# Kernel optimization log

Hardware: AMD Instinct MI355X
Metric: run time of the kernel (lower is better)

## Reference

```python
import jax, jax.numpy as jnp
import numpy as np

B, N, P_FEATS = 8, 4096, 3
WIDTH, HEADS, LAYERS, N_LAT = 768, 12, 8, 256
NUM_FREQS = 8
D_HEAD = WIDTH // HEADS
SCALE = 1.0 / np.sqrt(np.sqrt(D_HEAD))  # applied to q and k separately
IN_DIM = 3 * (1 + 2 * NUM_FREQS) + P_FEATS  # 54
EPS = 1e-5


def fourier_embed(pc):
    # pc: [B,N,3] -> [B,N,51] (include_input + sin/cos at freqs 2^0..2^7)
    freqs = (2.0 ** jnp.arange(NUM_FREQS)).astype(pc.dtype)
    ang = pc[..., None] * freqs  # [B,N,3,F]
    ang = ang.reshape(*pc.shape[:-1], 3 * NUM_FREQS)
    return jnp.concatenate([pc, jnp.sin(ang), jnp.cos(ang)], axis=-1)


def layernorm(x, s, b):
    mu = jnp.mean(x, axis=-1, keepdims=True)
    var = jnp.mean(jnp.square(x - mu), axis=-1, keepdims=True)
    return (x - mu) * jax.lax.rsqrt(var + EPS) * s + b


def mh_attn(q, k, v):
    # q: [B,T,H,C], k/v: [B,S,H,C]
    w = jnp.einsum('bthc,bshc->bhts', q * SCALE, k * SCALE)
    w = jax.nn.softmax(w.astype(jnp.float32), axis=-1).astype(q.dtype)
    out = jnp.einsum('bhts,bshc->bthc', w, v)
    return out.reshape(*q.shape[:2], -1)


def setup_inputs() -> dict:
    key = jax.random.key(0)
    ks = iter(jax.random.split(key, 64))
    rn = lambda shape, std=0.02: jax.random.normal(next(ks), shape, jnp.float32) * std
    inp = {
        'pc': jax.random.normal(next(ks), (B, N, 3), jnp.float32),
        'feats': jax.random.uniform(next(ks), (B, N, P_FEATS), jnp.float32),
        'query': rn((N_LAT, WIDTH)),
        'in_W': rn((WIDTH, IN_DIM)), 'in_b': jnp.zeros((WIDTH,)),
        'ca_qkv_W': rn((3 * WIDTH, WIDTH)), 'ca_qkv_b': jnp.zeros((3 * WIDTH,)),
        'ca_proj_W': rn((WIDTH, WIDTH)), 'ca_proj_b': jnp.zeros((WIDTH,)),
        'ln1_s': jnp.ones((LAYERS, WIDTH)), 'ln1_b': jnp.zeros((LAYERS, WIDTH)),
        'qkv_W': rn((LAYERS, 3 * WIDTH, WIDTH)), 'qkv_b': jnp.zeros((LAYERS, 3 * WIDTH)),
        'proj_W': rn((LAYERS, WIDTH, WIDTH)), 'proj_b': jnp.zeros((LAYERS, WIDTH)),
        'ln2_s': jnp.ones((LAYERS, WIDTH)), 'ln2_b': jnp.zeros((LAYERS, WIDTH)),
        'fc_W': rn((LAYERS, 4 * WIDTH, WIDTH)), 'fc_b': jnp.zeros((LAYERS, 4 * WIDTH)),
        'fc2_W': rn((LAYERS, WIDTH, 4 * WIDTH)), 'fc2_b': jnp.zeros((LAYERS, WIDTH)),
    }
    return inp


def _forward(pc, feats, query, in_W, in_b, ca_qkv_W, ca_qkv_b, ca_proj_W, ca_proj_b,
             ln1_s, ln1_b, qkv_W, qkv_b, proj_W, proj_b, ln2_s, ln2_b,
             fc_W, fc_b, fc2_W, fc2_b):
    bs = pc.shape[0]
    data = jnp.concatenate([fourier_embed(pc), feats], axis=-1)  # [B,N,54]
    data = data @ in_W.T + in_b  # [B,N,W]
    q_lat = jnp.broadcast_to(query[None], (bs, N_LAT, WIDTH))

    # --- cross attention (no residual, matching source) ---
    q = (q_lat @ ca_qkv_W.T + ca_qkv_b)[..., :WIDTH]
    kv = data @ ca_qkv_W.T + ca_qkv_b
    k, v = kv[..., WIDTH:2 * WIDTH], kv[..., 2 * WIDTH:]
    q = q.reshape(bs, N_LAT, HEADS, D_HEAD)
    k = k.reshape(bs, N, HEADS, D_HEAD)
    v = v.reshape(bs, N, HEADS, D_HEAD)
    latents = mh_attn(q, k, v) @ ca_proj_W.T + ca_proj_b  # [B,L,W]

    # --- self-attention transformer stack via scan ---
    def block(x, p):
        (l1s, l1b, qW, qb, pW, pb, l2s, l2b, fW, fb, f2W, f2b) = p
        h = layernorm(x, l1s, l1b)
        qkv = (h @ qW.T + qb).reshape(bs, N_LAT, HEADS, 3 * D_HEAD)
        qh, kh, vh = jnp.split(qkv, 3, axis=-1)
        x = x + mh_attn(qh, kh, vh) @ pW.T + pb
        h = layernorm(x, l2s, l2b)
        h = jax.nn.gelu(h @ fW.T + fb, approximate=False) @ f2W.T + f2b
        return x + h, None

    params = (ln1_s, ln1_b, qkv_W, qkv_b, proj_W, proj_b, ln2_s, ln2_b, fc_W, fc_b, fc2_W, fc2_b)
    latents, _ = jax.lax.scan(block, latents, params)
    return latents, pc


def reference(pc, feats, query, in_W, in_b, ca_qkv_W, ca_qkv_b, ca_proj_W, ca_proj_b,
              ln1_s, ln1_b, qkv_W, qkv_b, proj_W, proj_b, ln2_s, ln2_b,
              fc_W, fc_b, fc2_W, fc2_b):
    return _forward(pc, feats, query, in_W, in_b, ca_qkv_W, ca_qkv_b, ca_proj_W, ca_proj_b,
                    ln1_s, ln1_b, qkv_W, qkv_b, proj_W, proj_b, ln2_s, ln2_b,
                    fc_W, fc_b, fc2_W, fc2_b)
```

## Files before the change

kernel.cpp:

```cpp
#include <hip/hip_runtime.h>
#include <stdint.h>

typedef unsigned short u16;
typedef __bf16 bf16x8 __attribute__((ext_vector_type(8)));
typedef float f32x4 __attribute__((ext_vector_type(4)));

#define DEVINL __device__ __forceinline__

DEVINL u16 f2bf(float f) {
  union { float f; unsigned u; } c; c.f = f;
  unsigned u = c.u + 0x7FFFu + ((c.u >> 16) & 1u);
  return (u16)(u >> 16);
}

DEVINL float bf2f(u16 v) {
  union { unsigned u; float f; } c; c.u = (unsigned)v << 16;
  return c.f;
}

DEVINL unsigned pk2bf(float a, float b) {
#if __has_builtin(__builtin_amdgcn_cvt_pk_bf16_f32)
  auto r = __builtin_amdgcn_cvt_pk_bf16_f32(a, b);
  unsigned u;
  __builtin_memcpy(&u, &r, 4);
  return u;
#else
  return (unsigned)f2bf(a) | ((unsigned)f2bf(b) << 16);
#endif
}

DEVINL void gl2lds16(const void* g, void* l) {
  __builtin_amdgcn_global_load_lds(
      (const __attribute__((address_space(1))) unsigned int*)g,
      (__attribute__((address_space(3))) unsigned int*)l, 16, 0, 0);
}

DEVINL void waitlgkm0() { asm volatile("s_waitcnt lgkmcnt(0)" ::: "memory"); }
DEVINL void bar() {
  asm volatile("" ::: "memory");
  __builtin_amdgcn_s_barrier();
  asm volatile("" ::: "memory");
}

__global__ __launch_bounds__(256) void cvt4_kernel(
    const float* __restrict__ s0, u16* __restrict__ d0, int n0,
    const float* __restrict__ s1, u16* __restrict__ d1, int n1,
    const float* __restrict__ s2, u16* __restrict__ d2, int n2,
    const float* __restrict__ s3, u16* __restrict__ d3, int n3) {
  int i = blockIdx.x * 256 + threadIdx.x;
  const float* s; u16* d;
  if (i < n0) { s = s0; d = d0; }
  else {
    i -= n0;
    if (i < n1) { s = s1; d = d1; }
    else {
      i -= n1;
      if (i < n2) { s = s2; d = d2; }
      else {
        i -= n2;
        if (i >= n3) return;
        s = s3; d = d3;
      }
    }
  }
  float4 v = ((const float4*)s)[i];
  ((uint2*)d)[i] = make_uint2(pk2bf(v.x, v.y), pk2bf(v.z, v.w));
}

__global__ __launch_bounds__(256) void pad_inwT_kernel(const float* __restrict__ src,
                                                       u16* __restrict__ dst) {
  int t = blockIdx.x * 256 + threadIdx.x;
  if (t >= 64 * 768) return;
  int j = t / 768, o = t - j * 768;
  dst[t] = (j < 54) ? f2bf(src[o * 54 + j]) : (u16)0;
}

__global__ __launch_bounds__(256) void bprime_kernel(const float* __restrict__ caW,
                                                     const float* __restrict__ caB,
                                                     const float* __restrict__ inb,
                                                     float* __restrict__ bp) {
  int w = threadIdx.x >> 6, lane = threadIdx.x & 63;
  int m = blockIdx.x * 4 + w;
  const float* row = caW + (size_t)(768 + m) * 768;
  float s = 0.f;
#pragma unroll
  for (int k = 0; k < 12; k++) s += row[lane + k * 64] * inb[lane + k * 64];
#pragma unroll
  for (int msk = 32; msk >= 1; msk >>= 1) s += __shfl_xor(s, msk, 64);
  if (lane == 0) bp[m] = s + caB[768 + m];
}

__global__ __launch_bounds__(256) void embed_kernel(const float* __restrict__ pc,
                                                    const float* __restrict__ feats,
                                                    u16* __restrict__ emb) {
  int t = blockIdx.x * 256 + threadIdx.x;
  int p = t >> 6, c = t & 63;
  float v = 0.f;
  if (c < 3) {
    v = pc[p * 3 + c];
  } else if (c < 27) {
    int i = c - 3;
    float f = (float)(1 << (i & 7));
    v = sinf(pc[p * 3 + (i >> 3)] * f);
  } else if (c < 51) {
    int i = c - 27;
    float f = (float)(1 << (i & 7));
    v = cosf(pc[p * 3 + (i >> 3)] * f);
  } else if (c < 54) {
    v = feats[p * 3 + (c - 51)];
  }
  emb[t] = f2bf(v);
}

template <int TM, int TN, int WR, int WC, int MODE>
__global__ __launch_bounds__(256) void gemm_t(
    const u16* __restrict__ A, const u16* __restrict__ Bw,
    const float* __restrict__ bias, const float* __restrict__ resid,
    float* __restrict__ outF, u16* __restrict__ outB,
    int M, int N, int Nout, int K, int gelu,
    u16* __restrict__ vt, int vy, int skvt, int bsh) {
  constexpr int IM = TM / WR / 16;
  constexpr int IN = TN / WC / 16;
  __shared__ u16 As[TM * 32];
  __shared__ u16 Bs[TN * 32];
  const int tid = threadIdx.x;
  const int lane = tid & 63, w = tid >> 6;
  const int l15 = lane & 15, quad = lane >> 4;
  const int mblk = blockIdx.x * TM, nblk = blockIdx.y * TN;
  const int wm = (w % WR) * (TM / WR);
  const int wn = (w / WR) * (TN / WC);

  f32x4 acc[IM][IN];
#pragma unroll
  for (int i = 0; i < IM; i++)
#pragma unroll
    for (int j = 0; j < IN; j++) acc[i][j] = f32x4{0.f, 0.f, 0.f, 0.f};

  bool tv = false;
  if (MODE == 1) tv = ((int)blockIdx.y >= vy);
  if (MODE == 2) tv = ((int)(blockIdx.y % 3) == 2);

  if (!tv) {
    for (int k0 = 0; k0 < K; k0 += 32) {
#pragma unroll
      for (int s = tid; s < TM * 4; s += 256) {
        int row = s >> 2, c8 = (s & 3) << 3;
        gl2lds16(A + (size_t)(mblk + row) * K + (k0 + c8), &As[s * 8]);
      }
#pragma unroll
      for (int s = tid; s < TN * 4; s += 256) {
        int row = s >> 2, c8 = (s & 3) << 3;
        gl2lds16(Bw + (size_t)(nblk + row) * K + (k0 + c8), &Bs[s * 8]);
      }
      __syncthreads();
      bf16x8 af[IM], bfr[IN];
#pragma unroll
      for (int i = 0; i < IM; i++)
        af[i] = *(const bf16x8*)&As[(wm + i * 16 + l15) * 32 + quad * 8];
#pragma unroll
      for (int j = 0; j < IN; j++)
        bfr[j] = *(const bf16x8*)&Bs[(wn + j * 16 + l15) * 32 + quad * 8];
#pragma unroll
      for (int i = 0; i < IM; i++)
#pragma unroll
        for (int j = 0; j < IN; j++)
          acc[i][j] = __builtin_amdgcn_mfma_f32_16x16x32_bf16(bfr[j], af[i], acc[i][j], 0, 0, 0);
      __syncthreads();
    }
#pragma unroll
    for (int i = 0; i < IM; i++) {
      int m = mblk + wm + i * 16 + l15;
#pragma unroll
      for (int j = 0; j < IN; j++) {
        int n0 = nblk + wn + j * 16 + quad * 4;
        float4 bv = bias ? *(const float4*)&bias[n0] : make_float4(0.f, 0.f, 0.f, 0.f);
        float v0 = acc[i][j][0] + bv.x;
        float v1 = acc[i][j][1] + bv.y;
        float v2 = acc[i][j][2] + bv.z;
        float v3 = acc[i][j][3] + bv.w;
        if (gelu) {
          v0 = 0.5f * v0 * (1.0f + erff(v0 * 0.70710678118f));
          v1 = 0.5f * v1 * (1.0f + erff(v1 * 0.70710678118f));
          v2 = 0.5f * v2 * (1.0f + erff(v2 * 0.70710678118f));
          v3 = 0.5f * v3 * (1.0f + erff(v3 * 0.70710678118f));
        }
        size_t idx = (size_t)m * Nout + n0;
        if (resid) {
          float4 rv = *(const float4*)&resid[idx];
          v0 += rv.x; v1 += rv.y; v2 += rv.z; v3 += rv.w;
        }
        if (outF) {
          float4 ov = {v0, v1, v2, v3};
          *(float4*)&outF[idx] = ov;
        }
        if (outB) {
          *(uint2*)&outB[idx] = make_uint2(pk2bf(v0, v1), pk2bf(v2, v3));
        }
      }
    }
  } else {
    for (int k0 = 0; k0 < K; k0 += 32) {
#pragma unroll
      for (int s = tid; s < TM * 4; s += 256) {
        int row = s >> 2, c8 = (s & 3) << 3;
        gl2lds16(A + (size_t)(mblk + row) * K + (k0 + c8), &As[s * 8]);
      }
#pragma unroll
      for (int s = tid; s < TN * 4; s += 256) {
        int row = s >> 2, c8 = (s & 3) << 3;
        gl2lds16(Bw + (size_t)(nblk + row) * K + (k0 + c8), &Bs[s * 8]);
      }
      __syncthreads();
      bf16x8 af[IM], bfr[IN];
#pragma unroll
      for (int i = 0; i < IM; i++)
        af[i] = *(const bf16x8*)&As[(wm + i * 16 + l15) * 32 + quad * 8];
#pragma unroll
      for (int j = 0; j < IN; j++)
        bfr[j] = *(const bf16x8*)&Bs[(wn + j * 16 + l15) * 32 + quad * 8];
#pragma unroll
      for (int i = 0; i < IM; i++)
#pragma unroll
        for (int j = 0; j < IN; j++)
          acc[i][j] = __builtin_amdgcn_mfma_f32_16x16x32_bf16(af[i], bfr[j], acc[i][j], 0, 0, 0);
      __syncthreads();
    }
    int msk = (1 << bsh) - 1;
#pragma unroll
    for (int j = 0; j < IN; j++) {
      int n = nblk + wn + j * 16 + l15;
      float bv = bias ? bias[n] : 0.f;
#pragma unroll
      for (int i = 0; i < IM; i++) {
        int m0 = mblk + wm + i * 16 + quad * 4;
        int b = m0 >> bsh;
        int s0 = m0 & msk;
        float v0 = acc[i][j][0] + bv;
        float v1 = acc[i][j][1] + bv;
        float v2 = acc[i][j][2] + bv;
        float v3 = acc[i][j][3] + bv;
        size_t vrow;
        if (MODE == 2) {
          int h = blockIdx.y / 3;
          vrow = (size_t)(b * 12 + h) * 64 + (wn + j * 16 + l15);
        } else {
          vrow = (size_t)b * 768 + (n - vy * TN);
        }
        size_t addr = vrow * skvt + s0;
        *(uint2*)&vt[addr] = make_uint2(pk2bf(v0, v1), pk2bf(v2, v3));
      }
    }
  }
}

template <int TM, int TN, int WR, int WC>
__global__ __launch_bounds__(256) void gemmsk_t(
    const u16* __restrict__ A, const u16* __restrict__ Bw,
    float* __restrict__ P, int M, int N, int K, int kchunk) {
  constexpr int IM = TM / WR / 16;
  constexpr int IN = TN / WC / 16;
  __shared__ u16 As[TM * 32];
  __shared__ u16 Bs[TN * 32];
  const int tid = threadIdx.x;
  const int lane = tid & 63, w = tid >> 6;
  const int l15 = lane & 15, quad = lane >> 4;
  const int mblk = blockIdx.x * TM, nblk = blockIdx.y * TN;
  const int wm = (w % WR) * (TM / WR);
  const int wn = (w / WR) * (TN / WC);
  const int kbeg = blockIdx.z * kchunk;
  const int kend = kbeg + kchunk;

  f32x4 acc[IM][IN];
#pragma unroll
  for (int i = 0; i < IM; i++)
#pragma unroll
    for (int j = 0; j < IN; j++) acc[i][j] = f32x4{0.f, 0.f, 0.f, 0.f};

  for (int k0 = kbeg; k0 < kend; k0 += 32) {
#pragma unroll
    for (int s = tid; s < TM * 4; s += 256) {
      int row = s >> 2, c8 = (s & 3) << 3;
      gl2lds16(A + (size_t)(mblk + row) * K + (k0 + c8), &As[s * 8]);
    }
#pragma unroll
    for (int s = tid; s < TN * 4; s += 256) {
      int row = s >> 2, c8 = (s & 3) << 3;
      gl2lds16(Bw + (size_t)(nblk + row) * K + (k0 + c8), &Bs[s * 8]);
    }
    __syncthreads();
    bf16x8 af[IM], bfr[IN];
#pragma unroll
    for (int i = 0; i < IM; i++)
      af[i] = *(const bf16x8*)&As[(wm + i * 16 + l15) * 32 + quad * 8];
#pragma unroll
    for (int j = 0; j < IN; j++)
      bfr[j] = *(const bf16x8*)&Bs[(wn + j * 16 + l15) * 32 + quad * 8];
#pragma unroll
    for (int i = 0; i < IM; i++)
#pragma unroll
      for (int j = 0; j < IN; j++)
        acc[i][j] = __builtin_amdgcn_mfma_f32_16x16x32_bf16(bfr[j], af[i], acc[i][j], 0, 0, 0);
    __syncthreads();
  }

  float* Pz = P + (size_t)blockIdx.z * M * N;
#pragma unroll
  for (int i = 0; i < IM; i++) {
    int m = mblk + wm + i * 16 + l15;
#pragma unroll
    for (int j = 0; j < IN; j++) {
      int n0 = nblk + wn + j * 16 + quad * 4;
      float4 ov = {acc[i][j][0], acc[i][j][1], acc[i][j][2], acc[i][j][3]};
      *(float4*)&Pz[(size_t)m * N + n0] = ov;
    }
  }
}

__global__ __launch_bounds__(256) void skred_kernel(
    const float* __restrict__ P, int nsk, int MN4, int N,
    const float* __restrict__ bias, const float* __restrict__ resid,
    float* __restrict__ outF, u16* __restrict__ outB) {
  int i = blockIdx.x * 256 + threadIdx.x;
  if (i >= MN4) return;
  float4 s = ((const float4*)P)[i];
  for (int z = 1; z < nsk; z++) {
    float4 t = ((const float4*)P)[(size_t)z * MN4 + i];
    s.x += t.x; s.y += t.y; s.z += t.z; s.w += t.w;
  }
  if (bias) {
    int n0 = (i * 4) % N;
    float4 b = *(const float4*)&bias[n0];
    s.x += b.x; s.y += b.y; s.z += b.z; s.w += b.w;
  }
  if (resid) {
    float4 r = ((const float4*)resid)[i];
    s.x += r.x; s.y += r.y; s.z += r.z; s.w += r.w;
  }
  if (outF) ((float4*)outF)[i] = s;
  if (outB) ((uint2*)outB)[i] = make_uint2(pk2bf(s.x, s.y), pk2bf(s.z, s.w));
}

__global__ __launch_bounds__(256) void flash_kernel(
    const u16* __restrict__ Q, long qb, int qrs, int qhs,
    const u16* __restrict__ Kp, long kb, int krs, int khs,
    const u16* __restrict__ Vt, u16* __restrict__ Out,
    u16* __restrict__ Part, float* __restrict__ Ml,
    int Skv, int nsplit, int kvlen, int nbh, float scale2) {
  __shared__ u16 SH[64 * 72 + 2 * 64 * 64];
  u16* const Qs = SH;
  u16* const Ps = SH;
  u16* const Ks = SH + 64 * 72;
  u16* const Vs = SH + 64 * 72 + 64 * 64;

  const int tid = threadIdx.x;
  const int lane = tid & 63, w = tid >> 6;
  const int l15 = lane & 15, quad = lane >> 4;

  int bid = blockIdx.x;
  int grp = nbh * nsplit;
  int qt = bid / grp;
  int rem = bid - qt * grp;
  int bh = rem / nsplit;
  int split = rem - bh * nsplit;
  int h = bh % 12, b = bh / 12;

  const u16* Qbase = Q + (size_t)b * qb + (size_t)(qt * 64) * qrs + h * qhs;
  const u16* Kbase = Kp + (size_t)b * kb + (size_t)h * khs;
  const u16* Vbase = Vt + ((size_t)(b * 12 + h) * 64) * Skv;

  int kt0 = split * kvlen;

#pragma unroll
  for (int p = 0; p < 2; ++p) {
    int slot = tid + p * 256;
    int row = slot >> 3, c = slot & 7;
    int cg = (c - row) & 7;
    gl2lds16(Qbase + (size_t)row * qrs + cg * 8, &Qs[slot * 8]);
    gl2lds16(Kbase + (size_t)(kt0 + row) * krs + cg * 8, &Ks[slot * 8]);
    gl2lds16(Vbase + (size_t)row * Skv + kt0 + cg * 8, &Vs[slot * 8]);
  }
  __syncthreads();

  bf16x8 qa[2];
#pragma unroll
  for (int kk = 0; kk < 2; kk++)
    qa[kk] = *(const bf16x8*)&Qs[(w * 16 + l15) * 64 + ((kk * 4 + quad + l15) & 7) * 8];
  waitlgkm0();
  bar();

  f32x4 zero = {0.f, 0.f, 0.f, 0.f};
  f32x4 O[4];
#pragma unroll
  for (int d = 0; d < 4; d++) O[d] = zero;
  float m_i = -1e30f, l_i = 0.f;

  const int srow = tid >> 3;
  const int scg = ((tid & 7) - srow) & 7;

  for (int kt = kt0; kt < kt0 + kvlen; kt += 64) {
    bool hasnext = (kt + 64 < kt0 + kvlen);
    uint4 kreg0, kreg1, vreg0, vreg1;
    if (hasnext) {
      kreg0 = *(const uint4*)(Kbase + (size_t)(kt + 64 + srow) * krs + scg * 8);
      kreg1 = *(const uint4*)(Kbase + (size_t)(kt + 64 + srow + 32) * krs + scg * 8);
      vreg0 = *(const uint4*)(Vbase + (size_t)srow * Skv + (kt + 64) + scg * 8);
      vreg1 = *(const uint4*)(Vbase + (size_t)(srow + 32) * Skv + (kt + 64) + scg * 8);
    }

    f32x4 St[4];
#pragma unroll
    for (int j = 0; j < 4; j++) St[j] = zero;
#pragma unroll
    for (int kk = 0; kk < 2; kk++) {
#pragma unroll
      for (int j = 0; j < 4; j++) {
        bf16x8 kf = *(const bf16x8*)&Ks[(j * 16 + l15) * 64 + ((kk * 4 + quad + l15) & 7) * 8];
        St[j] = __builtin_amdgcn_mfma_f32_16x16x32_bf16(kf, qa[kk], St[j], 0, 0, 0);
      }
    }

    float mx = St[0][0];
#pragma unroll
    for (int j = 0; j < 4; j++)
#pragma unroll
      for (int r = 0; r < 4; r++) mx = fmaxf(mx, St[j][r]);
    mx = fmaxf(mx, __shfl_xor(mx, 16, 64));
    mx = fmaxf(mx, __shfl_xor(mx, 32, 64));
    mx *= scale2;

    bool skip = __all(mx <= m_i + 8.f);
    float al = 1.f;
    if (!skip) {
      float mnew = fmaxf(m_i, mx);
      al = __expf(m_i - mnew);
      m_i = mnew;
    }
    float mref = m_i;
    float sum = 0.f;
#pragma unroll
    for (int j = 0; j < 4; j++) {
      float p0 = __expf(fmaf(St[j][0], scale2, -mref));
      float p1 = __expf(fmaf(St[j][1], scale2, -mref));
      float p2 = __expf(fmaf(St[j][2], scale2, -mref));
      float p3 = __expf(fmaf(St[j][3], scale2, -mref));
      sum += (p0 + p1) + (p2 + p3);
      *(uint2*)&Ps[(w * 16 + l15) * 72 + j * 16 + quad * 4] =
          make_uint2(pk2bf(p0, p1), pk2bf(p2, p3));
    }
    sum += __shfl_xor(sum, 16, 64);
    sum += __shfl_xor(sum, 32, 64);

    if (skip) {
      l_i += sum;
    } else {
      l_i = l_i * al + sum;
      float a0 = __shfl(al, quad * 20 + 0, 64);
      float a1 = __shfl(al, quad * 20 + 1, 64);
      float a2 = __shfl(al, quad * 20 + 2, 64);
      float a3 = __shfl(al, quad * 20 + 3, 64);
#pragma unroll
      for (int d = 0; d < 4; d++) {
        O[d][0] *= a0; O[d][1] *= a1; O[d][2] *= a2; O[d][3] *= a3;
      }
    }
    waitlgkm0();
#pragma unroll
    for (int kk = 0; kk < 2; kk++) {
      bf16x8 pa = *(const bf16x8*)&Ps[(w * 16 + l15) * 72 + kk * 32 + quad * 8];
#pragma unroll
      for (int d = 0; d < 4; d++) {
        bf16x8 vf = *(const bf16x8*)&Vs[(d * 16 + l15) * 64 + ((kk * 4 + quad + l15) & 7) * 8];
        O[d] = __builtin_amdgcn_mfma_f32_16x16x32_bf16(pa, vf, O[d], 0, 0, 0);
      }
    }

    if (hasnext) {
      bar();
      *(uint4*)&Ks[tid * 8] = kreg0;
      *(uint4*)&Ks[(tid + 256) * 8] = kreg1;
      *(uint4*)&Vs[tid * 8] = vreg0;
      *(uint4*)&Vs[(tid + 256) * 8] = vreg1;
      waitlgkm0();
      bar();
    }
  }

  float l0 = __shfl(l_i, quad * 20 + 0, 64);
  float l1 = __shfl(l_i, quad * 20 + 1, 64);
  float l2 = __shfl(l_i, quad * 20 + 2, 64);
  float l3 = __shfl(l_i, quad * 20 + 3, 64);

  if (nsplit == 1) {
    float inv0 = 1.f / l0, inv1 = 1.f / l1, inv2 = 1.f / l2, inv3 = 1.f / l3;
    u16* Ob = Out + ((size_t)(b * 256 + qt * 64 + w * 16 + quad * 4)) * 768 + h * 64 + l15;
#pragma unroll
    for (int d = 0; d < 4; d++) {
      Ob[(size_t)0 * 768 + d * 16] = f2bf(O[d][0] * inv0);
      Ob[(size_t)1 * 768 + d * 16] = f2bf(O[d][1] * inv1);
      Ob[(size_t)2 * 768 + d * 16] = f2bf(O[d][2] * inv2);
      Ob[(size_t)3 * 768 + d * 16] = f2bf(O[d][3] * inv3);
    }
  } else {
    float m0 = __shfl(m_i, quad * 20 + 0, 64);
    float m1 = __shfl(m_i, quad * 20 + 1, 64);
    float m2 = __shfl(m_i, quad * 20 + 2, 64);
    float m3 = __shfl(m_i, quad * 20 + 3, 64);
    u16* Pb = Part + ((size_t)(bh * 4 + qt) * nsplit + split) * 4096;
    int rowb = w * 16 + quad * 4;
#pragma unroll
    for (int d = 0; d < 4; d++) {
      Pb[(rowb + 0) * 64 + d * 16 + l15] = f2bf(O[d][0]);
      Pb[(rowb + 1) * 64 + d * 16 + l15] = f2bf(O[d][1]);
      Pb[(rowb + 2) * 64 + d * 16 + l15] = f2bf(O[d][2]);
      Pb[(rowb + 3) * 64 + d * 16 + l15] = f2bf(O[d][3]);
    }
    if (l15 == 0) {
      float* MlB = Ml + ((size_t)(bh * 4 + qt) * nsplit + split) * 128;
      MlB[rowb + 0] = m0; MlB[rowb + 1] = m1; MlB[rowb + 2] = m2; MlB[rowb + 3] = m3;
      MlB[64 + rowb + 0] = l0; MlB[64 + rowb + 1] = l1;
      MlB[64 + rowb + 2] = l2; MlB[64 + rowb + 3] = l3;
    }
  }
}

__global__ __launch_bounds__(256) void freduce_kernel(
    const u16* __restrict__ Part, const float* __restrict__ Ml,
    u16* __restrict__ Out, int nsplit) {
  int bid = blockIdx.x;
  int qt = bid & 3, bh = bid >> 2;
  int h = bh % 12, b = bh / 12;
  int tid = threadIdx.x;
  int r = tid >> 2, dc = tid & 3;
  const float* mlb = Ml + (size_t)(bh * 4 + qt) * nsplit * 128;
  float M = -1e30f;
  for (int s = 0; s < nsplit; s++) M = fmaxf(M, mlb[s * 128 + r]);
  float L = 0.f;
  float accv[16];
#pragma unroll
  for (int i = 0; i < 16; i++) accv[i] = 0.f;
  const u16* pb = Part + (size_t)(bh * 4 + qt) * nsplit * 4096 + r * 64 + dc * 16;
  for (int s = 0; s < nsplit; s++) {
    float wgt = __expf(mlb[s * 128 + r] - M);
    L += wgt * mlb[s * 128 + 64 + r];
    u16 tmp[16];
    *(uint4*)tmp = *(const uint4*)(pb + s * 4096);
    *(uint4*)(tmp + 8) = *(const uint4*)(pb + s * 4096 + 8);
#pragma unroll
    for (int i = 0; i < 16; i++) accv[i] += wgt * bf2f(tmp[i]);
  }
  float inv = 1.f / L;
  unsigned ot[8];
#pragma unroll
  for (int i = 0; i < 8; i++)
    ot[i] = pk2bf(accv[2 * i] * inv, accv[2 * i + 1] * inv);
  u16* ob = Out + ((size_t)(b * 256 + qt * 64 + r)) * 768 + h * 64 + dc * 16;
  *(uint4*)ob = *(uint4*)ot;
  *(uint4*)(ob + 8) = *(uint4*)(ot + 4);
}

__global__ __launch_bounds__(256) void ln_kernel(const float* __restrict__ X,
                                                 const float* __restrict__ sc,
                                                 const float* __restrict__ bi,
                                                 u16* __restrict__ Hout) {
  int row = blockIdx.x;
  int tid = threadIdx.x;
  const float* x = X + (size_t)row * 768;
  float v0 = x[tid], v1 = x[tid + 256], v2 = x[tid + 512];
  float s = v0 + v1 + v2;
  float q = v0 * v0 + v1 * v1 + v2 * v2;
#pragma unroll
  for (int m = 1; m < 64; m <<= 1) {
    s += __shfl_xor(s, m, 64);
    q += __shfl_xor(q, m, 64);
  }
  __shared__ float rs[4], rq[4];
  if ((tid & 63) == 0) { rs[tid >> 6] = s; rq[tid >> 6] = q; }
  __syncthreads();
  s = rs[0] + rs[1] + rs[2] + rs[3];
  q = rq[0] + rq[1] + rq[2] + rq[3];
  float mu = s * (1.f / 768.f);
  float var = q * (1.f / 768.f) - mu * mu;
  float rstd = rsqrtf(var + 1e-5f);
  u16* ho = Hout + (size_t)row * 768;
  ho[tid]       = f2bf((v0 - mu) * rstd * sc[tid]       + bi[tid]);
  ho[tid + 256] = f2bf((v1 - mu) * rstd * sc[tid + 256] + bi[tid + 256]);
  ho[tid + 512] = f2bf((v2 - mu) * rstd * sc[tid + 512] + bi[tid + 512]);
}

__global__ __launch_bounds__(256) void copy4_kernel(const float* __restrict__ src,
                                                    float* __restrict__ dst, int n4) {
  int i = blockIdx.x * 256 + threadIdx.x;
  if (i < n4) ((float4*)dst)[i] = ((const float4*)src)[i];
}

extern "C" void kernel_launch(void* const* d_in, const int* in_sizes, int n_in,
                              void* d_out, int out_size, void* d_ws, size_t ws_size,
                              hipStream_t stream) {
  const float* pc        = (const float*)d_in[0];
  const float* feats     = (const float*)d_in[1];
  const float* query     = (const float*)d_in[2];
  const float* in_W      = (const float*)d_in[3];
  const float* in_b      = (const float*)d_in[4];
  const float* ca_qkv_W  = (const float*)d_in[5];
  const float* ca_qkv_b  = (const float*)d_in[6];
  const float* ca_proj_W = (const float*)d_in[7];
  const float* ca_proj_b = (const float*)d_in[8];
  const float* ln1_s     = (const float*)d_in[9];
  const float* ln1_b     = (const float*)d_in[10];
  const float* qkv_W     = (const float*)d_in[11];
  const float* qkv_b     = (const float*)d_in[12];
  const float* proj_W    = (const float*)d_in[13];
  const float* proj_b    = (const float*)d_in[14];
  const float* ln2_s     = (const float*)d_in[15];
  const float* ln2_b     = (const float*)d_in[16];
  const float* fc_W      = (const float*)d_in[17];
  const float* fc_b      = (const float*)d_in[18];
  const float* fc2_W     = (const float*)d_in[19];
  const float* fc2_b     = (const float*)d_in[20];

  char* base = (char*)d_ws;
  size_t off = 0;
  auto alloc = [&](size_t bytes) -> char* {
    char* p = base + off;
    off += (bytes + 255) & ~(size_t)255;
    return p;
  };

  u16* WqT     = (u16*)alloc(64 * 768 * 2);
  u16* Wquery  = (u16*)alloc(256 * 768 * 2);
  u16* Wcaqkv  = (u16*)alloc(2304 * 768 * 2);
  u16* Wcaproj = (u16*)alloc(768 * 768 * 2);
  u16* Wkp     = (u16*)alloc(1536 * 64 * 2);
  float* bprime = (float*)alloc(1536 * 4);
  u16* qc      = (u16*)alloc(256 * 768 * 2);
  u16* attn    = (u16*)alloc((size_t)2048 * 768 * 2);
  u16* hbuf    = (u16*)alloc((size_t)2048 * 768 * 2);
  char* uni    = alloc(13369344);
  u16* qkvb    = (u16*)uni;
  u16* VtS     = (u16*)(uni + 9437184);
  u16* fc1     = (u16*)uni;
  u16* Part    = (u16*)uni;
  float* Ml    = (float*)(uni + 12582912);

  size_t fixed_end = off;
  const size_t wAllSz = (size_t)8 * (2304 * 768 + 768 * 768 + 2 * 3072 * 768) * 2;
  auto crossSz = [](int cb) {
    return (size_t)cb * 4096 * 64 * 2 + 2 * ((size_t)cb * 4096 * 768 * 2);
  };

  bool allw; int CB;
  if (fixed_end + (wAllSz > crossSz(8) ? wAllSz : crossSz(8)) + 65536 <= ws_size) {
    allw = true;  CB = 8;
  } else if (fixed_end + 14155776 + crossSz(2) + 65536 <= ws_size) {
    allw = false; CB = 2;
  } else {
    allw = false; CB = 1;
  }

  u16 *WqkvB, *WprojB, *WfcB, *Wfc2B, *emb, *kvbK, *VtC;
  if (allw) {
    char* X = base + off;
    WqkvB  = (u16*)X;
    WprojB = WqkvB + (size_t)8 * 2304 * 768;
    WfcB   = WprojB + (size_t)8 * 768 * 768;
    Wfc2B  = WfcB + (size_t)8 * 3072 * 768;
    emb  = (u16*)X;
    kvbK = (u16*)(X + (size_t)CB * 4096 * 64 * 2);
    VtC  = (u16*)(X + (size_t)CB * 4096 * 64 * 2 + (size_t)CB * 4096 * 768 * 2);
    off = fixed_end + (wAllSz > crossSz(8) ? wAllSz : crossSz(8));
  } else {
    WqkvB  = (u16*)alloc(2304 * 768 * 2);
    WprojB = (u16*)alloc(768 * 768 * 2);
    WfcB   = (u16*)alloc(3072 * 768 * 2);
    Wfc2B  = (u16*)alloc((size_t)768 * 3072 * 2);
    emb  = (u16*)alloc((size_t)CB * 4096 * 64 * 2);
    kvbK = (u16*)alloc((size_t)CB * 4096 * 768 * 2);
    VtC  = (u16*)alloc((size_t)CB * 4096 * 768 * 2);
  }

  const size_t pb2048 = (size_t)2048 * 768 * 4;
  auto fits = [&](size_t bytes) { return off + bytes + 4096 <= ws_size; };
  int nsk_fc2 = fits(4 * pb2048) ? 4 : (fits(2 * pb2048) ? 2 : 1);
  int nsk_pr  = fits(2 * pb2048) ? 2 : 1;
  int nsk_qc  = fits((size_t)256 * 768 * 4 * 8) ? 8 : 1;
  float* skP  = (float*)(base + off);

  float* latents = (float*)d_out;
  const float scale2 = 0.125f;

  {
    int n0 = 256 * 768 / 4, n1 = 2304 * 768 / 4, n2 = 768 * 768 / 4;
    cvt4_kernel<<<(n0 + n1 + n2 + 255) / 256, 256, 0, stream>>>(
        query, Wquery, n0, ca_qkv_W, Wcaqkv, n1, ca_proj_W, Wcaproj, n2,
        nullptr, nullptr, 0);
  }
  pad_inwT_kernel<<<192, 256, 0, stream>>>(in_W, WqT);
  gemm_t<64, 64, 2, 2, 0><<<dim3(24, 1), 256, 0, stream>>>(
      Wcaqkv + (size_t)768 * 768, WqT, nullptr, nullptr, nullptr, Wkp,
      1536, 64, 64, 768, 0, nullptr, 0, 0, 0);
  bprime_kernel<<<384, 256, 0, stream>>>(ca_qkv_W, ca_qkv_b, in_b, bprime);

  if (nsk_qc > 1) {
    gemmsk_t<64, 64, 2, 2><<<dim3(4, 12, nsk_qc), 256, 0, stream>>>(
        Wquery, Wcaqkv, skP, 256, 768, 768, 768 / nsk_qc);
    skred_kernel<<<192, 256, 0, stream>>>(
        skP, nsk_qc, 256 * 768 / 4, 768, ca_qkv_b, nullptr, nullptr, qc);
  } else {
    gemm_t<64, 64, 2, 2, 0><<<dim3(4, 12), 256, 0, stream>>>(
        Wquery, Wcaqkv, ca_qkv_b, nullptr, nullptr, qc,
        256, 768, 768, 768, 0, nullptr, 0, 0, 0);
  }

  int nchunk = 8 / CB;
  for (int c = 0; c < nchunk; ++c) {
    int Mc = CB * 4096;
    const float* pc_c = pc + (size_t)c * Mc * 3;
    const float* ft_c = feats + (size_t)c * Mc * 3;
    embed_kernel<<<Mc / 4, 256, 0, stream>>>(pc_c, ft_c, emb);
    gemm_t<128, 128, 2, 2, 1><<<dim3(Mc / 128, 12), 256, 0, stream>>>(
        emb, Wkp, bprime, nullptr, nullptr, kvbK,
        Mc, 1536, 768, 64, 0, VtC, 6, 4096, 12);
    flash_kernel<<<CB * 12 * 16, 256, 0, stream>>>(
        qc, 0L, 768, 64, kvbK, (long)4096 * 768, 768, 64, VtC,
        nullptr, Part, Ml, 4096, 4, 1024, CB * 12, scale2);
    freduce_kernel<<<CB * 48, 256, 0, stream>>>(
        Part, Ml, attn + (size_t)c * CB * 256 * 768, 4);
  }
  if (nsk_pr > 1) {
    gemmsk_t<64, 64, 2, 2><<<dim3(32, 12, nsk_pr), 256, 0, stream>>>(
        attn, Wcaproj, skP, 2048, 768, 768, 768 / nsk_pr);
    skred_kernel<<<1536, 256, 0, stream>>>(
        skP, nsk_pr, 2048 * 768 / 4, 768, ca_proj_b, nullptr, latents, nullptr);
  } else {
    gemm_t<64, 64, 2, 2, 0><<<dim3(32, 12), 256, 0, stream>>>(
        attn, Wcaproj, ca_proj_b, nullptr, latents, nullptr,
        2048, 768, 768, 768, 0, nullptr, 0, 0, 0);
  }

  if (allw) {
    int n0 = 8 * 2304 * 768 / 4, n1 = 8 * 768 * 768 / 4, n2 = 8 * 3072 * 768 / 4;
    cvt4_kernel<<<(n0 + n1 + 2 * n2 + 255) / 256, 256, 0, stream>>>(
        qkv_W, WqkvB, n0, proj_W, WprojB, n1, fc_W, WfcB, n2, fc2_W, Wfc2B, n2);
  }

  for (int l = 0; l < 8; ++l) {
    u16* Wlq  = allw ? WqkvB  + (size_t)l * 2304 * 768 : WqkvB;
    u16* Wlp  = allw ? WprojB + (size_t)l * 768 * 768  : WprojB;
    u16* Wlf  = allw ? WfcB   + (size_t)l * 3072 * 768 : WfcB;
    u16* Wlf2 = allw ? Wfc2B  + (size_t)l * 3072 * 768 : Wfc2B;
    if (!allw) {
      int n0 = 2304 * 768 / 4, n1 = 768 * 768 / 4, n2 = 3072 * 768 / 4;
      cvt4_kernel<<<(n0 + n1 + 2 * n2 + 255) / 256, 256, 0, stream>>>(
          qkv_W + (size_t)l * 2304 * 768, Wlq, n0,
          proj_W + (size_t)l * 768 * 768, Wlp, n1,
          fc_W + (size_t)l * 3072 * 768, Wlf, n2,
          fc2_W + (size_t)l * 768 * 3072, Wlf2, n2);
    }
    ln_kernel<<<2048, 256, 0, stream>>>(latents, ln1_s + l * 768, ln1_b + l * 768, hbuf);
    gemm_t<64, 64, 2, 2, 2><<<dim3(32, 36), 256, 0, stream>>>(
        hbuf, Wlq, qkv_b + l * 2304, nullptr, nullptr, qkvb,
        2048, 2304, 2304, 768, 0, VtS, 0, 256, 8);
    flash_kernel<<<384, 256, 0, stream>>>(
        qkvb, (long)256 * 2304, 2304, 192, qkvb + 64, (long)256 * 2304, 2304, 192,
        VtS, attn, nullptr, nullptr, 256, 1, 256, 96, scale2);
    if (nsk_pr > 1) {
      gemmsk_t<64, 64, 2, 2><<<dim3(32, 12, nsk_pr), 256, 0, stream>>>(
          attn, Wlp, skP, 2048, 768, 768, 768 / nsk_pr);
      skred_kernel<<<1536, 256, 0, stream>>>(
          skP, nsk_pr, 2048 * 768 / 4, 768, proj_b + l * 768, latents, latents, nullptr);
    } else {
      gemm_t<64, 64, 2, 2, 0><<<dim3(32, 12), 256, 0, stream>>>(
          attn, Wlp, proj_b + l * 768, latents, latents, nullptr,
          2048, 768, 768, 768, 0, nullptr, 0, 0, 0);
    }
    ln_kernel<<<2048, 256, 0, stream>>>(latents, ln2_s + l * 768, ln2_b + l * 768, hbuf);
    gemm_t<64, 128, 1, 4, 0><<<dim3(32, 24), 256, 0, stream>>>(
        hbuf, Wlf, fc_b + l * 3072, nullptr, nullptr, fc1,
        2048, 3072, 3072, 768, 1, nullptr, 0, 0, 0);
    if (nsk_fc2 > 1) {
      gemmsk_t<64, 64, 2, 2><<<dim3(32, 12, nsk_fc2), 256, 0, stream>>>(
          fc1, Wlf2, skP, 2048, 768, 3072, 3072 / nsk_fc2);
      skred_kernel<<<1536, 256, 0, stream>>>(
          skP, nsk_fc2, 2048 * 768 / 4, 768, fc2_b + l * 768, latents, latents, nullptr);
    } else {
      gemm_t<64, 64, 2, 2, 0><<<dim3(32, 12), 256, 0, stream>>>(
          fc1, Wlf2, fc2_b + l * 768, latents, latents, nullptr,
          2048, 768, 768, 3072, 0, nullptr, 0, 0, 0);
    }
  }

  copy4_kernel<<<96, 256, 0, stream>>>(pc, (float*)d_out + (size_t)2048 * 768, 98304 / 4);
}
```

Before: 1.302 ms.

## Convert fc weights to bf16 inside GEMM staging instead of a separate pass

The fc and fc2 GEMMs now read fp32 weights directly and convert them to bf16 while staging into LDS, so the bulk conversion kernel no longer writes and rereads the bf16 copy of the two largest weight tensors. The conversion kernel is also changed to process 8 elements per thread in a grid-stride loop with a capped grid. The cost is that each GEMM tile now loads twice the weight bytes through registers rather than asynchronously with global_load_lds, and the weight tiles are reread by the 32 M-blocks, so weight traffic and VGPR pressure in the GEMM may rise.

```diff
diff --git a/kernel.cpp b/kernel.cpp
--- a/kernel.cpp
+++ b/kernel.cpp
@@ -42,29 +42,30 @@
   asm volatile("" ::: "memory");
 }
 
-__global__ __launch_bounds__(256) void cvt4_kernel(
+__global__ __launch_bounds__(256) void cvt8_kernel(
     const float* __restrict__ s0, u16* __restrict__ d0, int n0,
     const float* __restrict__ s1, u16* __restrict__ d1, int n1,
     const float* __restrict__ s2, u16* __restrict__ d2, int n2,
     const float* __restrict__ s3, u16* __restrict__ d3, int n3) {
-  int i = blockIdx.x * 256 + threadIdx.x;
-  const float* s; u16* d;
-  if (i < n0) { s = s0; d = d0; }
-  else {
-    i -= n0;
-    if (i < n1) { s = s1; d = d1; }
+  int ntot = n0 + n1 + n2 + n3;
+  for (int i = blockIdx.x * 256 + threadIdx.x; i < ntot; i += gridDim.x * 256) {
+    int j = i;
+    const float* s; u16* d;
+    if (j < n0) { s = s0; d = d0; }
     else {
-      i -= n1;
-      if (i < n2) { s = s2; d = d2; }
+      j -= n0;
+      if (j < n1) { s = s1; d = d1; }
       else {
-        i -= n2;
-        if (i >= n3) return;
-        s = s3; d = d3;
-      }
-    }
-  }
-  float4 v = ((const float4*)s)[i];
-  ((uint2*)d)[i] = make_uint2(pk2bf(v.x, v.y), pk2bf(v.z, v.w));
+        j -= n1;
+        if (j < n2) { s = s2; d = d2; }
+        else { j -= n2; s = s3; d = d3; }
+      }
+    }
+    const float4* sp = (const float4*)s + 2 * (size_t)j;
+    float4 a = sp[0], b = sp[1];
+    ((uint4*)d)[j] = make_uint4(pk2bf(a.x, a.y), pk2bf(a.z, a.w),
+                                pk2bf(b.x, b.y), pk2bf(b.z, b.w));
+  }
 }
 
 __global__ __launch_bounds__(256) void pad_inwT_kernel(const float* __restrict__ src,
@@ -112,7 +113,7 @@
   emb[t] = f2bf(v);
 }
 
-template <int TM, int TN, int WR, int WC, int MODE>
+template <int TM, int TN, int WR, int WC, int MODE, int BF32 = 0>
 __global__ __launch_bounds__(256) void gemm_t(
     const u16* __restrict__ A, const u16* __restrict__ Bw,
     const float* __restrict__ bias, const float* __restrict__ resid,
@@ -140,6 +141,27 @@
   if (MODE == 1) tv = ((int)blockIdx.y >= vy);
   if (MODE == 2) tv = ((int)(blockIdx.y % 3) == 2);
 
+  auto stageB = [&](int k0) {
+    if constexpr (BF32 != 0) {
+      const float* B32 = (const float*)Bw;
+#pragma unroll
+      for (int s = tid; s < TN * 4; s += 256) {
+        int row = s >> 2, c8 = (s & 3) << 3;
+        const float* src = B32 + (size_t)(nblk + row) * K + (k0 + c8);
+        float4 x = *(const float4*)src;
+        float4 y = *(const float4*)(src + 4);
+        *(uint4*)&Bs[s * 8] = make_uint4(pk2bf(x.x, x.y), pk2bf(x.z, x.w),
+                                         pk2bf(y.x, y.y), pk2bf(y.z, y.w));
+      }
+    } else {
+#pragma unroll
+      for (int s = tid; s < TN * 4; s += 256) {
+        int row = s >> 2, c8 = (s & 3) << 3;
+        gl2lds16(Bw + (size_t)(nblk + row) * K + (k0 + c8), &Bs[s * 8]);
+      }
+    }
+  };
+
   if (!tv) {
     for (int k0 = 0; k0 < K; k0 += 32) {
 #pragma unroll
@@ -147,11 +169,7 @@
         int row = s >> 2, c8 = (s & 3) << 3;
         gl2lds16(A + (size_t)(mblk + row) * K + (k0 + c8), &As[s * 8]);
       }
-#pragma unroll
-      for (int s = tid; s < TN * 4; s += 256) {
-        int row = s >> 2, c8 = (s & 3) << 3;
-        gl2lds16(Bw + (size_t)(nblk + row) * K + (k0 + c8), &Bs[s * 8]);
-      }
+      stageB(k0);
       __syncthreads();
       bf16x8 af[IM], bfr[IN];
 #pragma unroll
@@ -205,11 +223,7 @@
         int row = s >> 2, c8 = (s & 3) << 3;
         gl2lds16(A + (size_t)(mblk + row) * K + (k0 + c8), &As[s * 8]);
       }
-#pragma unroll
-      for (int s = tid; s < TN * 4; s += 256) {
-        int row = s >> 2, c8 = (s & 3) << 3;
-        gl2lds16(Bw + (size_t)(nblk + row) * K + (k0 + c8), &Bs[s * 8]);
-      }
+      stageB(k0);
       __syncthreads();
       bf16x8 af[IM], bfr[IN];
 #pragma unroll
@@ -253,7 +267,7 @@
   }
 }
 
-template <int TM, int TN, int WR, int WC>
+template <int TM, int TN, int WR, int WC, int BF32 = 0>
 __global__ __launch_bounds__(256) void gemmsk_t(
     const u16* __restrict__ A, const u16* __restrict__ Bw,
     float* __restrict__ P, int M, int N, int K, int kchunk) {
@@ -282,10 +296,23 @@
       int row = s >> 2, c8 = (s & 3) << 3;
       gl2lds16(A + (size_t)(mblk + row) * K + (k0 + c8), &As[s * 8]);
     }
-#pragma unroll
-    for (int s = tid; s < TN * 4; s += 256) {
-      int row = s >> 2, c8 = (s & 3) << 3;
-      gl2lds16(Bw + (size_t)(nblk + row) * K + (k0 + c8), &Bs[s * 8]);
+    if constexpr (BF32 != 0) {
+      const float* B32 = (const float*)Bw;
+#pragma unroll
+      for (int s = tid; s < TN * 4; s += 256) {
+        int row = s >> 2, c8 = (s & 3) << 3;
+        const float* src = B32 + (size_t)(nblk + row) * K + (k0 + c8);
+        float4 x = *(const float4*)src;
+        float4 y = *(const float4*)(src + 4);
+        *(uint4*)&Bs[s * 8] = make_uint4(pk2bf(x.x, x.y), pk2bf(x.z, x.w),
+                                         pk2bf(y.x, y.y), pk2bf(y.z, y.w));
+      }
+    } else {
+#pragma unroll
+      for (int s = tid; s < TN * 4; s += 256) {
+        int row = s >> 2, c8 = (s & 3) << 3;
+        gl2lds16(Bw + (size_t)(nblk + row) * K + (k0 + c8), &Bs[s * 8]);
+      }
     }
     __syncthreads();
     bf16x8 af[IM], bfr[IN];
@@ -643,7 +670,7 @@
   float* Ml    = (float*)(uni + 12582912);
 
   size_t fixed_end = off;
-  const size_t wAllSz = (size_t)8 * (2304 * 768 + 768 * 768 + 2 * 3072 * 768) * 2;
+  const size_t wAllSz = (size_t)8 * (2304 * 768 + 768 * 768) * 2;
   auto crossSz = [](int cb) {
     return (size_t)cb * 4096 * 64 * 2 + 2 * ((size_t)cb * 4096 * 768 * 2);
   };
@@ -651,19 +678,17 @@
   bool allw; int CB;
   if (fixed_end + (wAllSz > crossSz(8) ? wAllSz : crossSz(8)) + 65536 <= ws_size) {
     allw = true;  CB = 8;
-  } else if (fixed_end + 14155776 + crossSz(2) + 65536 <= ws_size) {
+  } else if (fixed_end + 4718592 + crossSz(2) + 65536 <= ws_size) {
     allw = false; CB = 2;
   } else {
     allw = false; CB = 1;
   }
 
-  u16 *WqkvB, *WprojB, *WfcB, *Wfc2B, *emb, *kvbK, *VtC;
+  u16 *WqkvB, *WprojB, *emb, *kvbK, *VtC;
   if (allw) {
     char* X = base + off;
     WqkvB  = (u16*)X;
     WprojB = WqkvB + (size_t)8 * 2304 * 768;
-    WfcB   = WprojB + (size_t)8 * 768 * 768;
-    Wfc2B  = WfcB + (size_t)8 * 3072 * 768;
     emb  = (u16*)X;
     kvbK = (u16*)(X + (size_t)CB * 4096 * 64 * 2);
     VtC  = (u16*)(X + (size_t)CB * 4096 * 64 * 2 + (size_t)CB * 4096 * 768 * 2);
@@ -671,8 +696,6 @@
   } else {
     WqkvB  = (u16*)alloc(2304 * 768 * 2);
     WprojB = (u16*)alloc(768 * 768 * 2);
-    WfcB   = (u16*)alloc(3072 * 768 * 2);
-    Wfc2B  = (u16*)alloc((size_t)768 * 3072 * 2);
     emb  = (u16*)alloc((size_t)CB * 4096 * 64 * 2);
     kvbK = (u16*)alloc((size_t)CB * 4096 * 768 * 2);
     VtC  = (u16*)alloc((size_t)CB * 4096 * 768 * 2);
@@ -689,8 +712,10 @@
   const float scale2 = 0.125f;
 
   {
-    int n0 = 256 * 768 / 4, n1 = 2304 * 768 / 4, n2 = 768 * 768 / 4;
-    cvt4_kernel<<<(n0 + n1 + n2 + 255) / 256, 256, 0, stream>>>(
+    int n0 = 256 * 768 / 8, n1 = 2304 * 768 / 8, n2 = 768 * 768 / 8;
+    int nt = n0 + n1 + n2;
+    int g = (nt + 255) / 256; if (g > 2048) g = 2048;
+    cvt8_kernel<<<g, 256, 0, stream>>>(
         query, Wquery, n0, ca_qkv_W, Wcaqkv, n1, ca_proj_W, Wcaproj, n2,
         nullptr, nullptr, 0);
   }
@@ -738,23 +763,24 @@
   }
 
   if (allw) {
-    int n0 = 8 * 2304 * 768 / 4, n1 = 8 * 768 * 768 / 4, n2 = 8 * 3072 * 768 / 4;
-    cvt4_kernel<<<(n0 + n1 + 2 * n2 + 255) / 256, 256, 0, stream>>>(
-        qkv_W, WqkvB, n0, proj_W, WprojB, n1, fc_W, WfcB, n2, fc2_W, Wfc2B, n2);
+    int n0 = 8 * 2304 * 768 / 8, n1 = 8 * 768 * 768 / 8;
+    cvt8_kernel<<<2048, 256, 0, stream>>>(
+        qkv_W, WqkvB, n0, proj_W, WprojB, n1, nullptr, nullptr, 0,
+        nullptr, nullptr, 0);
   }
 
   for (int l = 0; l < 8; ++l) {
     u16* Wlq  = allw ? WqkvB  + (size_t)l * 2304 * 768 : WqkvB;
     u16* Wlp  = allw ? WprojB + (size_t)l * 768 * 768  : WprojB;
-    u16* Wlf  = allw ? WfcB   + (size_t)l * 3072 * 768 : WfcB;
-    u16* Wlf2 = allw ? Wfc2B  + (size_t)l * 3072 * 768 : Wfc2B;
+    const u16* Wlf32  = (const u16*)(fc_W + (size_t)l * 3072 * 768);
+    const u16* Wlf232 = (const u16*)(fc2_W + (size_t)l * 768 * 3072);
     if (!allw) {
-      int n0 = 2304 * 768 / 4, n1 = 768 * 768 / 4, n2 = 3072 * 768 / 4;
-      cvt4_kernel<<<(n0 + n1 + 2 * n2 + 255) / 256, 256, 0, stream>>>(
+      int n0 = 2304 * 768 / 8, n1 = 768 * 768 / 8;
+      int g = (n0 + n1 + 255) / 256; if (g > 2048) g = 2048;
+      cvt8_kernel<<<g, 256, 0, stream>>>(
           qkv_W + (size_t)l * 2304 * 768, Wlq, n0,
           proj_W + (size_t)l * 768 * 768, Wlp, n1,
-          fc_W + (size_t)l * 3072 * 768, Wlf, n2,
-          fc2_W + (size_t)l * 768 * 3072, Wlf2, n2);
+          nullptr, nullptr, 0, nullptr, nullptr, 0);
     }
     ln_kernel<<<2048, 256, 0, stream>>>(latents, ln1_s + l * 768, ln1_b + l * 768, hbuf);
     gemm_t<64, 64, 2, 2, 2><<<dim3(32, 36), 256, 0, stream>>>(
@@ -774,17 +800,17 @@
           2048, 768, 768, 768, 0, nullptr, 0, 0, 0);
     }
     ln_kernel<<<2048, 256, 0, stream>>>(latents, ln2_s + l * 768, ln2_b + l * 768, hbuf);
-    gemm_t<64, 128, 1, 4, 0><<<dim3(32, 24), 256, 0, stream>>>(
-        hbuf, Wlf, fc_b + l * 3072, nullptr, nullptr, fc1,
+    gemm_t<64, 128, 1, 4, 0, 1><<<dim3(32, 24), 256, 0, stream>>>(
+        hbuf, Wlf32, fc_b + l * 3072, nullptr, nullptr, fc1,
         2048, 3072, 3072, 768, 1, nullptr, 0, 0, 0);
     if (nsk_fc2 > 1) {
-      gemmsk_t<64, 64, 2, 2><<<dim3(32, 12, nsk_fc2), 256, 0, stream>>>(
-          fc1, Wlf2, skP, 2048, 768, 3072, 3072 / nsk_fc2);
+      gemmsk_t<64, 64, 2, 2, 1><<<dim3(32, 12, nsk_fc2), 256, 0, stream>>>(
+          fc1, Wlf232, skP, 2048, 768, 3072, 3072 / nsk_fc2);
       skred_kernel<<<1536, 256, 0, stream>>>(
           skP, nsk_fc2, 2048 * 768 / 4, 768, fc2_b + l * 768, latents, latents, nullptr);
     } else {
-      gemm_t<64, 64, 2, 2, 0><<<dim3(32, 12), 256, 0, stream>>>(
-          fc1, Wlf2, fc2_b + l * 768, latents, latents, nullptr,
+      gemm_t<64, 64, 2, 2, 0, 1><<<dim3(32, 12), 256, 0, stream>>>(
+          fc1, Wlf232, fc2_b + l * 768, latents, latents, nullptr,
           2048, 768, 768, 3072, 0, nullptr, 0, 0, 0);
     }
   }
```

Result: slower. 1.538 ms (+18.1%).
